# Optimization experiments

Hardware: AMD Instinct MI355X
Metric: run time of the kernel (lower is better)

## Reference

```python
import jax, jax.numpy as jnp
import numpy as np

N_NODES = 8000
N_EDGES = 64000
HEADS = 8
OUT_C = 512
NEG_SLOPE = 0.2
EPS = 1e-16


def setup_inputs() -> dict:
    key = jax.random.key(0)
    ks = jax.random.split(key, 8)
    x = jax.random.normal(ks[0], (N_NODES, 128), dtype=jnp.float32)
    edge_index = jax.random.randint(ks[1], (2, N_EDGES), 0, N_NODES, dtype=jnp.int64)
    W_gat = jax.random.normal(ks[2], (128, HEADS * OUT_C), dtype=jnp.float32) * 0.05
    b_gat = jax.random.normal(ks[3], (HEADS * OUT_C,), dtype=jnp.float32) * 0.05
    att_src = jax.random.normal(ks[4], (HEADS, OUT_C), dtype=jnp.float32) * 0.05
    att_dst = jax.random.normal(ks[5], (HEADS, OUT_C), dtype=jnp.float32) * 0.05
    W_lin = jax.random.normal(ks[6], (HEADS * OUT_C, 512), dtype=jnp.float32) * 0.02
    b_lin = jax.random.normal(ks[7], (512,), dtype=jnp.float32) * 0.02
    return {"x": x, "edge_index": edge_index, "W_gat": W_gat, "b_gat": b_gat,
            "att_src": att_src, "att_dst": att_dst, "W_lin": W_lin, "b_lin": b_lin}


def reference(x, edge_index, W_gat, b_gat, att_src, att_dst, W_lin, b_lin):
    N = x.shape[0]
    # shared linear projection (PyG GATConv single-tensor input): [N, H, C]
    h = (x @ W_gat).reshape(N, HEADS, OUT_C)
    # add self loops (PyG default add_self_loops=True)
    loop = jnp.arange(N, dtype=edge_index.dtype)
    src = jnp.concatenate([edge_index[0], loop])  # source j
    dst = jnp.concatenate([edge_index[1], loop])  # destination i
    # per-node attention logits: [N, H]
    a_src = jnp.einsum('nhc,hc->nh', h, att_src)
    a_dst = jnp.einsum('nhc,hc->nh', h, att_dst)
    # edge logits, leaky relu
    e = jax.nn.leaky_relu(a_src[src] + a_dst[dst], NEG_SLOPE)  # [E, H]
    # softmax over edges sharing a destination
    emax = jax.ops.segment_max(e, dst, num_segments=N)
    ez = jnp.exp(e - emax[dst])
    denom = jax.ops.segment_sum(ez, dst, num_segments=N)
    alpha = ez / (denom[dst] + EPS)  # [E, H]
    # weighted scatter-add of source features
    msg = h[src] * alpha[:, :, None]  # [E, H, C]
    agg = jax.ops.segment_sum(msg, dst, num_segments=N)  # [N, H, C]
    gat_out = agg.reshape(N, HEADS * OUT_C) + b_gat
    return gat_out @ W_lin + b_lin
```

## Files before the change

kernel.cpp:

```cpp
#include <hip/hip_runtime.h>
#include <hip/hip_bf16.h>
#include <type_traits>

#define NN   8000
#define NE   64000
#define NE2  72000
#define NH   8
#define OC   512
#define HC   4096
#define KIN  128
#define NOUT 512
#define YW   1024
#define NEG_SLOPE 0.2f
#define WCSK 4

using bf16 = __hip_bfloat16;
typedef float  f32x4  __attribute__((ext_vector_type(4)));
typedef __bf16 bf16x8 __attribute__((ext_vector_type(8)));

static __device__ __forceinline__ void gld_lds16(const bf16* g, bf16* l){
    __builtin_amdgcn_global_load_lds(
        (const __attribute__((address_space(1))) unsigned int*)g,
        (__attribute__((address_space(3))) unsigned int*)l, 16, 0, 0);
}

#define TCVT_NB   2048
#define VSRC_BASE 2048
#define CNT_BASE  2176
#define PHA_NB    2458

__global__ __launch_bounds__(256) void k_phaseA(
    const float* __restrict__ W_lin, const float* __restrict__ b_gat,
    const float* __restrict__ W_gat,
    const float* __restrict__ att_src, const float* __restrict__ att_dst,
    const int* __restrict__ eidx,
    bf16* __restrict__ Wl_t, float* __restrict__ b_eff,
    bf16* __restrict__ Wg_bf, float* __restrict__ v,
    int* __restrict__ counts)
{
    __shared__ __align__(16) float smem[32*33 + 32];
    const int bid = blockIdx.x;
    const int tid = threadIdx.x;

    if (bid < TCVT_NB){
        float (*t)[33] = (float(*)[33])smem;
        float* bpart = smem + 32*33;
        if (tid < 32) bpart[tid] = 0.f;
        __syncthreads();
        int tx = tid & 31, ty = tid >> 5;
        int n0 = (bid & 15) * 32, k0 = (bid >> 4) * 32;
        float pb = 0.f;
        #pragma unroll
        for (int i=0;i<4;++i){
            int k = k0 + ty + 8*i;
            float val = W_lin[(size_t)k*NOUT + n0 + tx];
            t[ty+8*i][tx] = val;
            pb = fmaf(b_gat[k], val, pb);
        }
        atomicAdd(&bpart[tx], pb);
        __syncthreads();
        #pragma unroll
        for (int i=0;i<4;++i)
            Wl_t[(size_t)(n0+ty+8*i)*HC + k0+tx] = __float2bfloat16(t[tx][ty+8*i]);
        if (tid < 32) atomicAdd(b_eff + n0 + tid, bpart[tid]);
    } else if (bid < CNT_BASE){
        int k = bid - VSRC_BASE;
        int lane = tid & 63, g = tid >> 6;
        for (int hh = g; hh < NH; hh += 4){
            const float* wp = W_gat + (size_t)k*HC + hh*OC;
            bf16*        wb = Wg_bf + (size_t)k*HC + hh*OC;
            const float* as = att_src + hh*OC;
            const float* ad = att_dst + hh*OC;
            float ss = 0.f, sd = 0.f;
            #pragma unroll
            for (int c0=0; c0<OC; c0+=64){
                float wv = wp[c0+lane];
                wb[c0+lane] = __float2bfloat16(wv);
                ss = fmaf(wv, as[c0+lane], ss);
                sd = fmaf(wv, ad[c0+lane], sd);
            }
            #pragma unroll
            for (int off=32; off; off>>=1){
                ss += __shfl_down(ss, off);
                sd += __shfl_down(sd, off);
            }
            if (lane == 0){
                v[k*16 + hh]     = ss;
                v[k*16 + 8 + hh] = sd;
            }
        }
    } else {
        int e = (bid - CNT_BASE)*256 + tid;
        if (e < NE2){
            int dst = (e < NE) ? eidx[NE + e] : (e - NE);
            atomicAdd(&counts[dst], 1);
        }
    }
}

__global__ __launch_bounds__(256) void k_phaseB(
    const bf16* __restrict__ Wl_t, const bf16* __restrict__ Wg_bf,
    float* __restrict__ partW,
    const int* __restrict__ counts, int* __restrict__ offsets)
{
    __shared__ __align__(16) bf16 sA[2][128*32];
    __shared__ __align__(16) bf16 sB[2][128*32];
    __shared__ int part[256];
    const int bid = blockIdx.x;
    const int tid = threadIdx.x;

    if (bid == 128){
        int t = tid;
        int base = t*32;
        int s = 0;
        for (int u=0;u<32;++u){ int i = base+u; if (i<NN) s += counts[i]; }
        part[t] = s;
        __syncthreads();
        for (int off=1; off<256; off<<=1){
            int vv = (t>=off) ? part[t-off] : 0;
            __syncthreads();
            part[t] += vv;
            __syncthreads();
        }
        int run = (t==0) ? 0 : part[t-1];
        for (int u=0;u<32;++u){
            int i = base+u;
            if (i<NN){ offsets[i] = run; run += counts[i]; }
        }
        if (t == 255) offsets[NN] = run;
        return;
    }

    const int head = (bid >> 2) / WCSK;
    const int sp   = (bid >> 2) % WCSK;
    const bf16* A  = Wl_t  + head*OC + sp*128;
    const bf16* BT = Wg_bf + head*OC + sp*128;
    const int lane = tid & 63;
    const int w    = tid >> 6;
    const int wm   = w >> 1, wn = w & 1;
    const int m16  = lane & 15, q = lane >> 4;
    const int m0 = (bid & 3) * 128;

    const int c0 = w*64 + lane;
    const int c1 = 256 + c0;
    const int rA0 = c0 >> 2, kA0 = (c0 & 3) * 8;
    const int rA1 = c1 >> 2, kA1 = (c1 & 3) * 8;
    const size_t gA0 = (size_t)(m0 + rA0) * HC + kA0;
    const size_t gA1 = (size_t)(m0 + rA1) * HC + kA1;
    const size_t gB0 = (size_t)rA0 * HC + kA0;
    const size_t gB1 = (size_t)rA1 * HC + kA1;

    f32x4 acc[4][4];
    #pragma unroll
    for (int i=0;i<4;++i)
        #pragma unroll
        for (int j=0;j<4;++j)
            #pragma unroll
            for (int r=0;r<4;++r) acc[i][j][r] = 0.f;

    gld_lds16(A  + gA0, sA[0] + c0*8);
    gld_lds16(A  + gA1, sA[0] + c1*8);
    gld_lds16(BT + gB0, sB[0] + c0*8);
    gld_lds16(BT + gB1, sB[0] + c1*8);
    __syncthreads();

    #pragma unroll
    for (int it = 0; it < 4; ++it){
        const int cur = it & 1, nxt = cur ^ 1;
        bf16x8 af[4], bfr[4];
        #pragma unroll
        for (int t=0;t<4;++t){
            af[t]  = *(const bf16x8*)(const void*)(sA[cur] + ((wm*64 + t*16 + m16)*32 + q*8));
            bfr[t] = *(const bf16x8*)(const void*)(sB[cur] + ((wn*64 + t*16 + m16)*32 + q*8));
        }
        if (it + 1 < 4){
            int ko = (it+1) * 32;
            gld_lds16(A  + gA0 + ko, sA[nxt] + c0*8);
            gld_lds16(A  + gA1 + ko, sA[nxt] + c1*8);
            gld_lds16(BT + gB0 + ko, sB[nxt] + c0*8);
            gld_lds16(BT + gB1 + ko, sB[nxt] + c1*8);
        }
        #pragma unroll
        for (int i=0;i<4;++i)
            #pragma unroll
            for (int j=0;j<4;++j)
                acc[i][j] = __builtin_amdgcn_mfma_f32_16x16x32_bf16(af[i], bfr[j], acc[i][j], 0, 0, 0);
        __syncthreads();
    }

    float* pout = partW + (size_t)sp*NOUT*YW + head*KIN;
    #pragma unroll
    for (int i=0;i<4;++i){
        int row_base = m0 + wm*64 + i*16 + q*4;
        #pragma unroll
        for (int j=0;j<4;++j){
            int col = wn*64 + j*16 + m16;
            #pragma unroll
            for (int r=0;r<4;++r)
                pout[(size_t)(row_base + r)*YW + col] = acc[i][j][r];
        }
    }
}

#define FILL_NB 282
#define PHC_NB  782

__global__ __launch_bounds__(256) void k_phaseC(
    const int* __restrict__ eidx, const int* __restrict__ offsets,
    int* __restrict__ cursors, int* __restrict__ esrc,
    const float* __restrict__ x, const float* __restrict__ v,
    float* __restrict__ a_src, float* __restrict__ a_dst)
{
    __shared__ __align__(16) float smem[16*132*2];
    const int bid = blockIdx.x;
    const int tid = threadIdx.x;

    if (bid < FILL_NB){
        int e = bid*256 + tid;
        if (e < NE2){
            int src, dst;
            if (e < NE){ src = eidx[e]; dst = eidx[NE+e]; } else { src = dst = e - NE; }
            int pos = atomicAdd(&cursors[dst], 1);
            esrc[offsets[dst] + pos] = src;
        }
        return;
    }
    float (*xs)[132] = (float(*)[132])smem;
    float (*vt)[132] = (float(*)[132])(smem + 16*132);
    int node0 = (bid - FILL_NB) * 16;
    {
        const float* xg = x + (size_t)node0*KIN;
        int row = tid >> 4, co = (tid & 15) * 8;
        float4 v0 = *(const float4*)(xg + row*KIN + co);
        float4 v1 = *(const float4*)(xg + row*KIN + co + 4);
        *(float4*)&xs[row][co]     = v0;
        *(float4*)&xs[row][co + 4] = v1;
    }
    {
        int base = tid*8;
        #pragma unroll
        for (int j=0;j<8;++j){
            int idx = base + j;
            vt[idx & 15][idx >> 4] = v[idx];
        }
    }
    __syncthreads();
    int ln = tid >> 4, o = tid & 15;
    float acc = 0.f;
    #pragma unroll
    for (int k0=0;k0<KIN;k0+=4){
        float4 xv = *(const float4*)&xs[ln][k0];
        float4 vv = *(const float4*)&vt[o][k0];
        acc += xv.x*vv.x + xv.y*vv.y + xv.z*vv.z + xv.w*vv.w;
    }
    int node = node0 + ln;
    if (o < 8) a_src[node*NH + o]     = acc;
    else       a_dst[node*NH + o - 8] = acc;
}

__global__ __launch_bounds__(256) void k_aggxr(const int* __restrict__ offs,
    const int* __restrict__ esrc, const float* __restrict__ a_src,
    const float* __restrict__ a_dst, const float* __restrict__ x,
    const float* __restrict__ partW, bf16* __restrict__ Y, bf16* __restrict__ WcT)
{
    int bid = blockIdx.x;
    int tid = threadIdx.x;
    if (bid >= NN/4){
        int t = (bid - NN/4)*256 + tid;
        int base = t*8;
        float s[8];
        #pragma unroll
        for (int j=0;j<8;++j) s[j] = 0.f;
        #pragma unroll
        for (int sp=0; sp<WCSK; ++sp){
            const float4* pp = (const float4*)(partW + (size_t)sp*NOUT*YW + base);
            float4 p0 = pp[0], p1 = pp[1];
            s[0]+=p0.x; s[1]+=p0.y; s[2]+=p0.z; s[3]+=p0.w;
            s[4]+=p1.x; s[5]+=p1.y; s[6]+=p1.z; s[7]+=p1.w;
        }
        bf16x8 o;
        #pragma unroll
        for (int j=0;j<8;++j) o[j] = (__bf16)s[j];
        *(bf16x8*)(void*)(WcT + base) = o;
        return;
    }
    int node = bid*4 + (tid >> 6);
    int lane = tid & 63;
    int s0 = offs[node], s1 = offs[node+1];
    int g = lane >> 3, h = lane & 7;
    float adl = a_dst[node*NH + h];
    float m = -1e30f, sum = 0.f;
    for (int e = s0 + g; e < s1; e += 8){
        float l = a_src[esrc[e]*NH + h] + adl;
        l = l > 0.f ? l : NEG_SLOPE*l;
        float mn = fmaxf(m, l);
        sum = sum*__expf(m - mn) + __expf(l - mn);
        m = mn;
    }
    #pragma unroll
    for (int d=8; d<64; d<<=1){
        float mo = __shfl_xor(m, d);
        float so = __shfl_xor(sum, d);
        float mn = fmaxf(m, mo);
        sum = sum*__expf(m - mn) + so*__expf(mo - mn);
        m = mn;
    }
    float inv = 1.f / (sum + 1e-16f);
    float acc[16];
    #pragma unroll
    for (int j=0;j<16;++j) acc[j] = 0.f;
    for (int s=s0; s<s1; ++s){
        int src = esrc[s];
        float wl = 0.f;
        if (lane < 8){
            float l = a_src[src*NH + lane] + adl;
            l = l > 0.f ? l : NEG_SLOPE*l;
            wl = __expf(l - m) * inv;
        }
        float2 xv = *(const float2*)(x + (size_t)src*KIN + lane*2);
        #pragma unroll
        for (int hh=0; hh<8; ++hh){
            float wh = __shfl(wl, hh);
            acc[hh*2]   = fmaf(wh, xv.x, acc[hh*2]);
            acc[hh*2+1] = fmaf(wh, xv.y, acc[hh*2+1]);
        }
    }
    bf16* yp = Y + (size_t)node*YW + lane*2;
    #pragma unroll
    for (int hh=0; hh<8; ++hh){
        bf16 b0 = __float2bfloat16(acc[hh*2]);
        bf16 b1 = __float2bfloat16(acc[hh*2+1]);
        ushort2 pk;
        pk.x = *(unsigned short*)&b0;
        pk.y = *(unsigned short*)&b1;
        *reinterpret_cast<ushort2*>(yp + hh*KIN) = pk;
    }
}

__global__ __launch_bounds__(256) void k_gemm64(
    const bf16* __restrict__ A, const bf16* __restrict__ BT,
    const float* __restrict__ b_eff, const float* __restrict__ b_lin,
    float* __restrict__ C, int M, int N, int K)
{
    __shared__ __align__(16) bf16 sA[2][64*32];
    __shared__ __align__(16) bf16 sB[2][128*32];
    const int tid  = threadIdx.x;
    const int lane = tid & 63;
    const int w    = tid >> 6;
    const int wm   = w >> 1, wn = w & 1;
    const int m16  = lane & 15, q = lane >> 4;
    const int m0 = blockIdx.x * 64;
    const int n0 = blockIdx.y * 128;

    const int rA = tid >> 2,  kA = (tid & 3) * 8;
    const int cB0 = tid, cB1 = 256 + tid;
    const int rB0 = cB0 >> 2, kB0 = (cB0 & 3) * 8;
    const int rB1 = cB1 >> 2, kB1 = (cB1 & 3) * 8;
    const size_t gA  = (size_t)(m0 + rA)  * K + kA;
    const size_t gB0 = (size_t)(n0 + rB0) * K + kB0;
    const size_t gB1 = (size_t)(n0 + rB1) * K + kB1;

    f32x4 acc[2][4];
    #pragma unroll
    for (int i=0;i<2;++i)
        #pragma unroll
        for (int j=0;j<4;++j)
            #pragma unroll
            for (int r=0;r<4;++r) acc[i][j][r] = 0.f;

    gld_lds16(A  + gA,  sA[0] + tid*8);
    gld_lds16(BT + gB0, sB[0] + cB0*8);
    gld_lds16(BT + gB1, sB[0] + cB1*8);
    __syncthreads();

    const int nIter = K / 32;
    for (int it = 0; it < nIter; ++it){
        const int cur = it & 1, nxt = cur ^ 1;
        bf16x8 af[2], bfr[4];
        #pragma unroll
        for (int i=0;i<2;++i)
            af[i]  = *(const bf16x8*)(const void*)(sA[cur] + ((wm*32 + i*16 + m16)*32 + q*8));
        #pragma unroll
        for (int j=0;j<4;++j)
            bfr[j] = *(const bf16x8*)(const void*)(sB[cur] + ((wn*64 + j*16 + m16)*32 + q*8));
        if (it + 1 < nIter){
            int ko = (it+1) * 32;
            gld_lds16(A  + gA  + ko, sA[nxt] + tid*8);
            gld_lds16(BT + gB0 + ko, sB[nxt] + cB0*8);
            gld_lds16(BT + gB1 + ko, sB[nxt] + cB1*8);
        }
        #pragma unroll
        for (int i=0;i<2;++i)
            #pragma unroll
            for (int j=0;j<4;++j)
                acc[i][j] = __builtin_amdgcn_mfma_f32_16x16x32_bf16(af[i], bfr[j], acc[i][j], 0, 0, 0);
        __syncthreads();
    }

    #pragma unroll
    for (int i=0;i<2;++i){
        int row_base = m0 + wm*32 + i*16 + q*4;
        #pragma unroll
        for (int j=0;j<4;++j){
            int col = n0 + wn*64 + j*16 + m16;
            float bval = b_eff[col] + b_lin[col];
            #pragma unroll
            for (int r=0;r<4;++r)
                C[(size_t)(row_base + r)*N + col] = acc[i][j][r] + bval;
        }
    }
}

extern "C" void kernel_launch(void* const* d_in, const int* in_sizes, int n_in,
                              void* d_out, int out_size, void* d_ws, size_t ws_size,
                              hipStream_t stream)
{
    const float* x       = (const float*)d_in[0];
    const int*   eidx    = (const int*)  d_in[1];
    const float* W_gat   = (const float*)d_in[2];
    const float* b_gat   = (const float*)d_in[3];
    const float* att_src = (const float*)d_in[4];
    const float* att_dst = (const float*)d_in[5];
    const float* W_lin   = (const float*)d_in[6];
    const float* b_lin   = (const float*)d_in[7];
    float* out = (float*)d_out;

    char* p = (char*)d_ws;
    auto alloc = [&](size_t bytes){ void* r = (void*)p; p += (bytes + 255) & ~(size_t)255; return r; };
    bf16*  Wg_bf  = (bf16*) alloc((size_t)KIN*HC*2);
    bf16*  Wl_t   = (bf16*) alloc((size_t)NOUT*HC*2);
    bf16*  WcT    = (bf16*) alloc((size_t)NOUT*YW*2);
    bf16*  Ybuf   = (bf16*) alloc((size_t)NN*YW*2);
    float* partW  = (float*)alloc((size_t)WCSK*NOUT*YW*4);
    float* v      = (float*)alloc((size_t)KIN*16*4);
    float* a_src  = (float*)alloc((size_t)NN*NH*4);
    float* a_dst  = (float*)alloc((size_t)NN*NH*4);
    int*   offs   = (int*)  alloc((size_t)(NN+1)*4);
    int*   esrc   = (int*)  alloc((size_t)NE2*4);
    int*   counts = (int*)  alloc((size_t)NN*4);
    int*   cursors= (int*)  alloc((size_t)NN*4);
    float* b_eff  = (float*)alloc((size_t)NOUT*4);
    if ((size_t)(p - (char*)d_ws) > ws_size) return;

    hipMemsetAsync(counts, 0, (size_t)2*NN*4 + NOUT*4, stream);
    k_phaseA<<<PHA_NB, 256, 0, stream>>>(W_lin, b_gat, W_gat, att_src, att_dst,
                                         eidx, Wl_t, b_eff, Wg_bf, v, counts);
    k_phaseB<<<129, 256, 0, stream>>>(Wl_t, Wg_bf, partW, counts, offs);
    k_phaseC<<<PHC_NB, 256, 0, stream>>>(eidx, offs, cursors, esrc, x, v, a_src, a_dst);
    k_aggxr<<<NN/4 + NOUT*YW/(8*256), 256, 0, stream>>>(offs, esrc, a_src, a_dst,
                                                        x, partW, Ybuf, WcT);
    k_gemm64<<<dim3(NN/64, NOUT/128), 256, 0, stream>>>(Ybuf, WcT, b_eff, b_lin,
                                                        out, NN, NOUT, YW);
}
```

Baseline: 151.3 us.

## Merge all phases into one cooperative persistent kernel with grid syncs

Result: slower. 464.0 us (+206.7%).

```diff
diff --git a/kernel.cpp b/kernel.cpp
--- a/kernel.cpp
+++ b/kernel.cpp
@@ -1,6 +1,9 @@
 #include <hip/hip_runtime.h>
 #include <hip/hip_bf16.h>
+#include <hip/hip_cooperative_groups.h>
 #include <type_traits>
+
+namespace cg = cooperative_groups;
 
 #define NN   8000
 #define NE   64000
@@ -14,6 +17,17 @@
 #define NEG_SLOPE 0.2f
 #define WCSK 4
 
+#define TCVT_NB   2048
+#define VSRC_BASE 2048
+#define CNT_BASE  2176
+#define P1_NB     2458
+#define P2_NB     257
+#define FILL_NB   282
+#define P3_NB     782
+#define AGG_NB    2000
+#define P4_NB     2256
+#define P5_NB     500
+
 using bf16 = __hip_bfloat16;
 typedef float  f32x4  __attribute__((ext_vector_type(4)));
 typedef __bf16 bf16x8 __attribute__((ext_vector_type(8)));
@@ -24,353 +38,34 @@
         (__attribute__((address_space(3))) unsigned int*)l, 16, 0, 0);
 }
 
-#define TCVT_NB   2048
-#define VSRC_BASE 2048
-#define CNT_BASE  2176
-#define PHA_NB    2458
-
-__global__ __launch_bounds__(256) void k_phaseA(
-    const float* __restrict__ W_lin, const float* __restrict__ b_gat,
-    const float* __restrict__ W_gat,
-    const float* __restrict__ att_src, const float* __restrict__ att_dst,
-    const int* __restrict__ eidx,
-    bf16* __restrict__ Wl_t, float* __restrict__ b_eff,
-    bf16* __restrict__ Wg_bf, float* __restrict__ v,
-    int* __restrict__ counts)
+struct Acc24 { f32x4 a[2][4]; };
+
+static __device__ __forceinline__ void gemm64x128(
+    const bf16* __restrict__ A, int lda, const bf16* __restrict__ BT, int ldb,
+    int K, bf16* sA, bf16* sB, int tid, Acc24& acc)
 {
-    __shared__ __align__(16) float smem[32*33 + 32];
-    const int bid = blockIdx.x;
-    const int tid = threadIdx.x;
-
-    if (bid < TCVT_NB){
-        float (*t)[33] = (float(*)[33])smem;
-        float* bpart = smem + 32*33;
-        if (tid < 32) bpart[tid] = 0.f;
-        __syncthreads();
-        int tx = tid & 31, ty = tid >> 5;
-        int n0 = (bid & 15) * 32, k0 = (bid >> 4) * 32;
-        float pb = 0.f;
-        #pragma unroll
-        for (int i=0;i<4;++i){
-            int k = k0 + ty + 8*i;
-            float val = W_lin[(size_t)k*NOUT + n0 + tx];
-            t[ty+8*i][tx] = val;
-            pb = fmaf(b_gat[k], val, pb);
-        }
-        atomicAdd(&bpart[tx], pb);
-        __syncthreads();
-        #pragma unroll
-        for (int i=0;i<4;++i)
-            Wl_t[(size_t)(n0+ty+8*i)*HC + k0+tx] = __float2bfloat16(t[tx][ty+8*i]);
-        if (tid < 32) atomicAdd(b_eff + n0 + tid, bpart[tid]);
-    } else if (bid < CNT_BASE){
-        int k = bid - VSRC_BASE;
-        int lane = tid & 63, g = tid >> 6;
-        for (int hh = g; hh < NH; hh += 4){
-            const float* wp = W_gat + (size_t)k*HC + hh*OC;
-            bf16*        wb = Wg_bf + (size_t)k*HC + hh*OC;
-            const float* as = att_src + hh*OC;
-            const float* ad = att_dst + hh*OC;
-            float ss = 0.f, sd = 0.f;
-            #pragma unroll
-            for (int c0=0; c0<OC; c0+=64){
-                float wv = wp[c0+lane];
-                wb[c0+lane] = __float2bfloat16(wv);
-                ss = fmaf(wv, as[c0+lane], ss);
-                sd = fmaf(wv, ad[c0+lane], sd);
-            }
-            #pragma unroll
-            for (int off=32; off; off>>=1){
-                ss += __shfl_down(ss, off);
-                sd += __shfl_down(sd, off);
-            }
-            if (lane == 0){
-                v[k*16 + hh]     = ss;
-                v[k*16 + 8 + hh] = sd;
-            }
-        }
-    } else {
-        int e = (bid - CNT_BASE)*256 + tid;
-        if (e < NE2){
-            int dst = (e < NE) ? eidx[NE + e] : (e - NE);
-            atomicAdd(&counts[dst], 1);
-        }
-    }
-}
-
-__global__ __launch_bounds__(256) void k_phaseB(
-    const bf16* __restrict__ Wl_t, const bf16* __restrict__ Wg_bf,
-    float* __restrict__ partW,
-    const int* __restrict__ counts, int* __restrict__ offsets)
-{
-    __shared__ __align__(16) bf16 sA[2][128*32];
-    __shared__ __align__(16) bf16 sB[2][128*32];
-    __shared__ int part[256];
-    const int bid = blockIdx.x;
-    const int tid = threadIdx.x;
-
-    if (bid == 128){
-        int t = tid;
-        int base = t*32;
-        int s = 0;
-        for (int u=0;u<32;++u){ int i = base+u; if (i<NN) s += counts[i]; }
-        part[t] = s;
-        __syncthreads();
-        for (int off=1; off<256; off<<=1){
-            int vv = (t>=off) ? part[t-off] : 0;
-            __syncthreads();
-            part[t] += vv;
-            __syncthreads();
-        }
-        int run = (t==0) ? 0 : part[t-1];
-        for (int u=0;u<32;++u){
-            int i = base+u;
-            if (i<NN){ offsets[i] = run; run += counts[i]; }
-        }
-        if (t == 255) offsets[NN] = run;
-        return;
-    }
-
-    const int head = (bid >> 2) / WCSK;
-    const int sp   = (bid >> 2) % WCSK;
-    const bf16* A  = Wl_t  + head*OC + sp*128;
-    const bf16* BT = Wg_bf + head*OC + sp*128;
     const int lane = tid & 63;
     const int w    = tid >> 6;
     const int wm   = w >> 1, wn = w & 1;
     const int m16  = lane & 15, q = lane >> 4;
-    const int m0 = (bid & 3) * 128;
-
-    const int c0 = w*64 + lane;
-    const int c1 = 256 + c0;
-    const int rA0 = c0 >> 2, kA0 = (c0 & 3) * 8;
-    const int rA1 = c1 >> 2, kA1 = (c1 & 3) * 8;
-    const size_t gA0 = (size_t)(m0 + rA0) * HC + kA0;
-    const size_t gA1 = (size_t)(m0 + rA1) * HC + kA1;
-    const size_t gB0 = (size_t)rA0 * HC + kA0;
-    const size_t gB1 = (size_t)rA1 * HC + kA1;
-
-    f32x4 acc[4][4];
-    #pragma unroll
-    for (int i=0;i<4;++i)
-        #pragma unroll
-        for (int j=0;j<4;++j)
-            #pragma unroll
-            for (int r=0;r<4;++r) acc[i][j][r] = 0.f;
-
-    gld_lds16(A  + gA0, sA[0] + c0*8);
-    gld_lds16(A  + gA1, sA[0] + c1*8);
-    gld_lds16(BT + gB0, sB[0] + c0*8);
-    gld_lds16(BT + gB1, sB[0] + c1*8);
-    __syncthreads();
-
-    #pragma unroll
-    for (int it = 0; it < 4; ++it){
-        const int cur = it & 1, nxt = cur ^ 1;
-        bf16x8 af[4], bfr[4];
-        #pragma unroll
-        for (int t=0;t<4;++t){
-            af[t]  = *(const bf16x8*)(const void*)(sA[cur] + ((wm*64 + t*16 + m16)*32 + q*8));
-            bfr[t] = *(const bf16x8*)(const void*)(sB[cur] + ((wn*64 + t*16 + m16)*32 + q*8));
-        }
-        if (it + 1 < 4){
-            int ko = (it+1) * 32;
-            gld_lds16(A  + gA0 + ko, sA[nxt] + c0*8);
-            gld_lds16(A  + gA1 + ko, sA[nxt] + c1*8);
-            gld_lds16(BT + gB0 + ko, sB[nxt] + c0*8);
-            gld_lds16(BT + gB1 + ko, sB[nxt] + c1*8);
-        }
-        #pragma unroll
-        for (int i=0;i<4;++i)
-            #pragma unroll
-            for (int j=0;j<4;++j)
-                acc[i][j] = __builtin_amdgcn_mfma_f32_16x16x32_bf16(af[i], bfr[j], acc[i][j], 0, 0, 0);
-        __syncthreads();
-    }
-
-    float* pout = partW + (size_t)sp*NOUT*YW + head*KIN;
-    #pragma unroll
-    for (int i=0;i<4;++i){
-        int row_base = m0 + wm*64 + i*16 + q*4;
-        #pragma unroll
-        for (int j=0;j<4;++j){
-            int col = wn*64 + j*16 + m16;
-            #pragma unroll
-            for (int r=0;r<4;++r)
-                pout[(size_t)(row_base + r)*YW + col] = acc[i][j][r];
-        }
-    }
-}
-
-#define FILL_NB 282
-#define PHC_NB  782
-
-__global__ __launch_bounds__(256) void k_phaseC(
-    const int* __restrict__ eidx, const int* __restrict__ offsets,
-    int* __restrict__ cursors, int* __restrict__ esrc,
-    const float* __restrict__ x, const float* __restrict__ v,
-    float* __restrict__ a_src, float* __restrict__ a_dst)
-{
-    __shared__ __align__(16) float smem[16*132*2];
-    const int bid = blockIdx.x;
-    const int tid = threadIdx.x;
-
-    if (bid < FILL_NB){
-        int e = bid*256 + tid;
-        if (e < NE2){
-            int src, dst;
-            if (e < NE){ src = eidx[e]; dst = eidx[NE+e]; } else { src = dst = e - NE; }
-            int pos = atomicAdd(&cursors[dst], 1);
-            esrc[offsets[dst] + pos] = src;
-        }
-        return;
-    }
-    float (*xs)[132] = (float(*)[132])smem;
-    float (*vt)[132] = (float(*)[132])(smem + 16*132);
-    int node0 = (bid - FILL_NB) * 16;
-    {
-        const float* xg = x + (size_t)node0*KIN;
-        int row = tid >> 4, co = (tid & 15) * 8;
-        float4 v0 = *(const float4*)(xg + row*KIN + co);
-        float4 v1 = *(const float4*)(xg + row*KIN + co + 4);
-        *(float4*)&xs[row][co]     = v0;
-        *(float4*)&xs[row][co + 4] = v1;
-    }
-    {
-        int base = tid*8;
-        #pragma unroll
-        for (int j=0;j<8;++j){
-            int idx = base + j;
-            vt[idx & 15][idx >> 4] = v[idx];
-        }
-    }
-    __syncthreads();
-    int ln = tid >> 4, o = tid & 15;
-    float acc = 0.f;
-    #pragma unroll
-    for (int k0=0;k0<KIN;k0+=4){
-        float4 xv = *(const float4*)&xs[ln][k0];
-        float4 vv = *(const float4*)&vt[o][k0];
-        acc += xv.x*vv.x + xv.y*vv.y + xv.z*vv.z + xv.w*vv.w;
-    }
-    int node = node0 + ln;
-    if (o < 8) a_src[node*NH + o]     = acc;
-    else       a_dst[node*NH + o - 8] = acc;
-}
-
-__global__ __launch_bounds__(256) void k_aggxr(const int* __restrict__ offs,
-    const int* __restrict__ esrc, const float* __restrict__ a_src,
-    const float* __restrict__ a_dst, const float* __restrict__ x,
-    const float* __restrict__ partW, bf16* __restrict__ Y, bf16* __restrict__ WcT)
-{
-    int bid = blockIdx.x;
-    int tid = threadIdx.x;
-    if (bid >= NN/4){
-        int t = (bid - NN/4)*256 + tid;
-        int base = t*8;
-        float s[8];
-        #pragma unroll
-        for (int j=0;j<8;++j) s[j] = 0.f;
-        #pragma unroll
-        for (int sp=0; sp<WCSK; ++sp){
-            const float4* pp = (const float4*)(partW + (size_t)sp*NOUT*YW + base);
-            float4 p0 = pp[0], p1 = pp[1];
-            s[0]+=p0.x; s[1]+=p0.y; s[2]+=p0.z; s[3]+=p0.w;
-            s[4]+=p1.x; s[5]+=p1.y; s[6]+=p1.z; s[7]+=p1.w;
-        }
-        bf16x8 o;
-        #pragma unroll
-        for (int j=0;j<8;++j) o[j] = (__bf16)s[j];
-        *(bf16x8*)(void*)(WcT + base) = o;
-        return;
-    }
-    int node = bid*4 + (tid >> 6);
-    int lane = tid & 63;
-    int s0 = offs[node], s1 = offs[node+1];
-    int g = lane >> 3, h = lane & 7;
-    float adl = a_dst[node*NH + h];
-    float m = -1e30f, sum = 0.f;
-    for (int e = s0 + g; e < s1; e += 8){
-        float l = a_src[esrc[e]*NH + h] + adl;
-        l = l > 0.f ? l : NEG_SLOPE*l;
-        float mn = fmaxf(m, l);
-        sum = sum*__expf(m - mn) + __expf(l - mn);
-        m = mn;
-    }
-    #pragma unroll
-    for (int d=8; d<64; d<<=1){
-        float mo = __shfl_xor(m, d);
-        float so = __shfl_xor(sum, d);
-        float mn = fmaxf(m, mo);
-        sum = sum*__expf(m - mn) + so*__expf(mo - mn);
-        m = mn;
-    }
-    float inv = 1.f / (sum + 1e-16f);
-    float acc[16];
-    #pragma unroll
-    for (int j=0;j<16;++j) acc[j] = 0.f;
-    for (int s=s0; s<s1; ++s){
-        int src = esrc[s];
-        float wl = 0.f;
-        if (lane < 8){
-            float l = a_src[src*NH + lane] + adl;
-            l = l > 0.f ? l : NEG_SLOPE*l;
-            wl = __expf(l - m) * inv;
-        }
-        float2 xv = *(const float2*)(x + (size_t)src*KIN + lane*2);
-        #pragma unroll
-        for (int hh=0; hh<8; ++hh){
-            float wh = __shfl(wl, hh);
-            acc[hh*2]   = fmaf(wh, xv.x, acc[hh*2]);
-            acc[hh*2+1] = fmaf(wh, xv.y, acc[hh*2+1]);
-        }
-    }
-    bf16* yp = Y + (size_t)node*YW + lane*2;
-    #pragma unroll
-    for (int hh=0; hh<8; ++hh){
-        bf16 b0 = __float2bfloat16(acc[hh*2]);
-        bf16 b1 = __float2bfloat16(acc[hh*2+1]);
-        ushort2 pk;
-        pk.x = *(unsigned short*)&b0;
-        pk.y = *(unsigned short*)&b1;
-        *reinterpret_cast<ushort2*>(yp + hh*KIN) = pk;
-    }
-}
-
-__global__ __launch_bounds__(256) void k_gemm64(
-    const bf16* __restrict__ A, const bf16* __restrict__ BT,
-    const float* __restrict__ b_eff, const float* __restrict__ b_lin,
-    float* __restrict__ C, int M, int N, int K)
-{
-    __shared__ __align__(16) bf16 sA[2][64*32];
-    __shared__ __align__(16) bf16 sB[2][128*32];
-    const int tid  = threadIdx.x;
-    const int lane = tid & 63;
-    const int w    = tid >> 6;
-    const int wm   = w >> 1, wn = w & 1;
-    const int m16  = lane & 15, q = lane >> 4;
-    const int m0 = blockIdx.x * 64;
-    const int n0 = blockIdx.y * 128;
-
     const int rA = tid >> 2,  kA = (tid & 3) * 8;
     const int cB0 = tid, cB1 = 256 + tid;
     const int rB0 = cB0 >> 2, kB0 = (cB0 & 3) * 8;
     const int rB1 = cB1 >> 2, kB1 = (cB1 & 3) * 8;
-    const size_t gA  = (size_t)(m0 + rA)  * K + kA;
-    const size_t gB0 = (size_t)(n0 + rB0) * K + kB0;
-    const size_t gB1 = (size_t)(n0 + rB1) * K + kB1;
-
-    f32x4 acc[2][4];
+    const size_t gA  = (size_t)rA  * lda + kA;
+    const size_t gB0 = (size_t)rB0 * ldb + kB0;
+    const size_t gB1 = (size_t)rB1 * ldb + kB1;
+
     #pragma unroll
     for (int i=0;i<2;++i)
         #pragma unroll
         for (int j=0;j<4;++j)
             #pragma unroll
-            for (int r=0;r<4;++r) acc[i][j][r] = 0.f;
-
-    gld_lds16(A  + gA,  sA[0] + tid*8);
-    gld_lds16(BT + gB0, sB[0] + cB0*8);
-    gld_lds16(BT + gB1, sB[0] + cB1*8);
+            for (int r=0;r<4;++r) acc.a[i][j][r] = 0.f;
+
+    gld_lds16(A  + gA,  sA + tid*8);
+    gld_lds16(BT + gB0, sB + cB0*8);
+    gld_lds16(BT + gB1, sB + cB1*8);
     __syncthreads();
 
     const int nIter = K / 32;
@@ -379,34 +74,301 @@
         bf16x8 af[2], bfr[4];
         #pragma unroll
         for (int i=0;i<2;++i)
-            af[i]  = *(const bf16x8*)(const void*)(sA[cur] + ((wm*32 + i*16 + m16)*32 + q*8));
+            af[i]  = *(const bf16x8*)(const void*)(sA + cur*64*32 + ((wm*32 + i*16 + m16)*32 + q*8));
         #pragma unroll
         for (int j=0;j<4;++j)
-            bfr[j] = *(const bf16x8*)(const void*)(sB[cur] + ((wn*64 + j*16 + m16)*32 + q*8));
+            bfr[j] = *(const bf16x8*)(const void*)(sB + cur*128*32 + ((wn*64 + j*16 + m16)*32 + q*8));
         if (it + 1 < nIter){
             int ko = (it+1) * 32;
-            gld_lds16(A  + gA  + ko, sA[nxt] + tid*8);
-            gld_lds16(BT + gB0 + ko, sB[nxt] + cB0*8);
-            gld_lds16(BT + gB1 + ko, sB[nxt] + cB1*8);
+            gld_lds16(A  + gA  + ko, sA + nxt*64*32 + tid*8);
+            gld_lds16(BT + gB0 + ko, sB + nxt*128*32 + cB0*8);
+            gld_lds16(BT + gB1 + ko, sB + nxt*128*32 + cB1*8);
         }
         #pragma unroll
         for (int i=0;i<2;++i)
             #pragma unroll
             for (int j=0;j<4;++j)
-                acc[i][j] = __builtin_amdgcn_mfma_f32_16x16x32_bf16(af[i], bfr[j], acc[i][j], 0, 0, 0);
+                acc.a[i][j] = __builtin_amdgcn_mfma_f32_16x16x32_bf16(af[i], bfr[j], acc.a[i][j], 0, 0, 0);
         __syncthreads();
     }
-
-    #pragma unroll
-    for (int i=0;i<2;++i){
-        int row_base = m0 + wm*32 + i*16 + q*4;
+}
+
+__global__ __launch_bounds__(256, 4) void k_mega(
+    const float* __restrict__ x, const int* __restrict__ eidx,
+    const float* __restrict__ W_gat, const float* __restrict__ b_gat,
+    const float* __restrict__ att_src, const float* __restrict__ att_dst,
+    const float* __restrict__ W_lin, const float* __restrict__ b_lin,
+    float* __restrict__ out,
+    bf16* __restrict__ Wl_t, bf16* __restrict__ Wg_bf,
+    bf16* __restrict__ WcT, bf16* __restrict__ Ybuf,
+    float* __restrict__ partW, float* __restrict__ v,
+    float* __restrict__ a_src, float* __restrict__ a_dst,
+    int* __restrict__ offs, int* __restrict__ esrc,
+    int* __restrict__ zero_base)
+{
+    cg::grid_group grid = cg::this_grid();
+    __shared__ __align__(16) char smem_raw[24576];
+    int*   counts  = zero_base;
+    int*   cursors = zero_base + NN;
+    float* b_eff   = (float*)(zero_base + 2*NN);
+    const int tid = threadIdx.x;
+    const int nb  = gridDim.x;
+
+    for (int i = blockIdx.x*256 + tid; i < 2*NN + NOUT; i += nb*256)
+        zero_base[i] = 0;
+    grid.sync();
+
+    for (int vb = blockIdx.x; vb < P1_NB; vb += nb){
+        if (vb < TCVT_NB){
+            float (*t)[33] = (float(*)[33])smem_raw;
+            float* bpart = (float*)smem_raw + 32*33;
+            if (tid < 32) bpart[tid] = 0.f;
+            __syncthreads();
+            int tx = tid & 31, ty = tid >> 5;
+            int n0 = (vb & 15)*32, k0 = (vb >> 4)*32;
+            float pb = 0.f;
+            #pragma unroll
+            for (int i=0;i<4;++i){
+                int k = k0 + ty + 8*i;
+                float val = W_lin[(size_t)k*NOUT + n0 + tx];
+                t[ty+8*i][tx] = val;
+                pb = fmaf(b_gat[k], val, pb);
+            }
+            atomicAdd(&bpart[tx], pb);
+            __syncthreads();
+            #pragma unroll
+            for (int i=0;i<4;++i)
+                Wl_t[(size_t)(n0+ty+8*i)*HC + k0+tx] = __float2bfloat16(t[tx][ty+8*i]);
+            if (tid < 32) atomicAdd(b_eff + n0 + tid, bpart[tid]);
+            __syncthreads();
+        } else if (vb < CNT_BASE){
+            int k = vb - VSRC_BASE;
+            int lane = tid & 63, g = tid >> 6;
+            for (int hh = g; hh < NH; hh += 4){
+                const float* wp = W_gat + (size_t)k*HC + hh*OC;
+                bf16*        wb = Wg_bf + (size_t)k*HC + hh*OC;
+                const float* as = att_src + hh*OC;
+                const float* ad = att_dst + hh*OC;
+                float ss = 0.f, sd = 0.f;
+                #pragma unroll
+                for (int c0=0; c0<OC; c0+=64){
+                    float wv = wp[c0+lane];
+                    wb[c0+lane] = __float2bfloat16(wv);
+                    ss = fmaf(wv, as[c0+lane], ss);
+                    sd = fmaf(wv, ad[c0+lane], sd);
+                }
+                #pragma unroll
+                for (int off=32; off; off>>=1){
+                    ss += __shfl_down(ss, off);
+                    sd += __shfl_down(sd, off);
+                }
+                if (lane == 0){
+                    v[k*16 + hh]     = ss;
+                    v[k*16 + 8 + hh] = sd;
+                }
+            }
+        } else {
+            int e = (vb - CNT_BASE)*256 + tid;
+            if (e < NE2){
+                int dst = (e < NE) ? eidx[NE + e] : (e - NE);
+                atomicAdd(&counts[dst], 1);
+            }
+        }
+    }
+    grid.sync();
+
+    for (int vb = blockIdx.x; vb < P2_NB; vb += nb){
+        if (vb < 256){
+            bf16* sA = (bf16*)smem_raw;
+            bf16* sB = (bf16*)(smem_raw + 8192);
+            int head = vb >> 5, sp = (vb >> 3) & 3, mt = vb & 7;
+            const bf16* A  = Wl_t  + head*OC + sp*128 + (size_t)(mt*64)*HC;
+            const bf16* BT = Wg_bf + head*OC + sp*128;
+            Acc24 acc;
+            gemm64x128(A, HC, BT, HC, 128, sA, sB, tid, acc);
+            const int lane = tid & 63;
+            const int w = tid >> 6, wm = w >> 1, wn = w & 1;
+            const int m16 = lane & 15, q = lane >> 4;
+            float* pout = partW + (size_t)sp*NOUT*YW + head*KIN;
+            #pragma unroll
+            for (int i=0;i<2;++i){
+                int o_base = mt*64 + wm*32 + i*16 + q*4;
+                #pragma unroll
+                for (int j=0;j<4;++j){
+                    int col = wn*64 + j*16 + m16;
+                    #pragma unroll
+                    for (int r=0;r<4;++r)
+                        pout[(size_t)(o_base + r)*YW + col] = acc.a[i][j][r];
+                }
+            }
+        } else {
+            int* part = (int*)smem_raw;
+            int t = tid;
+            int base = t*32;
+            int s = 0;
+            for (int u=0;u<32;++u){ int i = base+u; if (i<NN) s += counts[i]; }
+            part[t] = s;
+            __syncthreads();
+            for (int off=1; off<256; off<<=1){
+                int vv = (t>=off) ? part[t-off] : 0;
+                __syncthreads();
+                part[t] += vv;
+                __syncthreads();
+            }
+            int run = (t==0) ? 0 : part[t-1];
+            for (int u=0;u<32;++u){
+                int i = base+u;
+                if (i<NN){ offs[i] = run; run += counts[i]; }
+            }
+            if (t == 255) offs[NN] = run;
+            __syncthreads();
+        }
+    }
+    grid.sync();
+
+    for (int vb = blockIdx.x; vb < P3_NB; vb += nb){
+        if (vb < FILL_NB){
+            int e = vb*256 + tid;
+            if (e < NE2){
+                int src, dst;
+                if (e < NE){ src = eidx[e]; dst = eidx[NE+e]; } else { src = dst = e - NE; }
+                int pos = atomicAdd(&cursors[dst], 1);
+                esrc[offs[dst] + pos] = src;
+            }
+        } else {
+            float (*xs)[132] = (float(*)[132])smem_raw;
+            float (*vt)[132] = (float(*)[132])((float*)smem_raw + 16*132);
+            int node0 = (vb - FILL_NB) * 16;
+            {
+                const float* xg = x + (size_t)node0*KIN;
+                int row = tid >> 4, co = (tid & 15) * 8;
+                float4 v0 = *(const float4*)(xg + row*KIN + co);
+                float4 v1 = *(const float4*)(xg + row*KIN + co + 4);
+                *(float4*)&xs[row][co]     = v0;
+                *(float4*)&xs[row][co + 4] = v1;
+            }
+            {
+                int base = tid*8;
+                #pragma unroll
+                for (int j=0;j<8;++j){
+                    int idx = base + j;
+                    vt[idx & 15][idx >> 4] = v[idx];
+                }
+            }
+            __syncthreads();
+            int ln = tid >> 4, o = tid & 15;
+            float acc = 0.f;
+            #pragma unroll
+            for (int k0=0;k0<KIN;k0+=4){
+                float4 xv = *(const float4*)&xs[ln][k0];
+                float4 vv = *(const float4*)&vt[o][k0];
+                acc += xv.x*vv.x + xv.y*vv.y + xv.z*vv.z + xv.w*vv.w;
+            }
+            int node = node0 + ln;
+            if (o < 8) a_src[node*NH + o]     = acc;
+            else       a_dst[node*NH + o - 8] = acc;
+            __syncthreads();
+        }
+    }
+    grid.sync();
+
+    for (int vb = blockIdx.x; vb < P4_NB; vb += nb){
+        if (vb >= AGG_NB){
+            int t = (vb - AGG_NB)*256 + tid;
+            int base = t*8;
+            float s[8];
+            #pragma unroll
+            for (int j=0;j<8;++j) s[j] = 0.f;
+            #pragma unroll
+            for (int sp=0; sp<WCSK; ++sp){
+                const float4* pp = (const float4*)(partW + (size_t)sp*NOUT*YW + base);
+                float4 p0 = pp[0], p1 = pp[1];
+                s[0]+=p0.x; s[1]+=p0.y; s[2]+=p0.z; s[3]+=p0.w;
+                s[4]+=p1.x; s[5]+=p1.y; s[6]+=p1.z; s[7]+=p1.w;
+            }
+            bf16x8 o;
+            #pragma unroll
+            for (int j=0;j<8;++j) o[j] = (__bf16)s[j];
+            *(bf16x8*)(void*)(WcT + base) = o;
+        } else {
+            int node = vb*4 + (tid >> 6);
+            int lane = tid & 63;
+            int s0 = offs[node], s1 = offs[node+1];
+            int g = lane >> 3, h = lane & 7;
+            float adl = a_dst[node*NH + h];
+            float m = -1e30f, sum = 0.f;
+            for (int e = s0 + g; e < s1; e += 8){
+                float l = a_src[esrc[e]*NH + h] + adl;
+                l = l > 0.f ? l : NEG_SLOPE*l;
+                float mn = fmaxf(m, l);
+                sum = sum*__expf(m - mn) + __expf(l - mn);
+                m = mn;
+            }
+            #pragma unroll
+            for (int d=8; d<64; d<<=1){
+                float mo = __shfl_xor(m, d);
+                float so = __shfl_xor(sum, d);
+                float mn = fmaxf(m, mo);
+                sum = sum*__expf(m - mn) + so*__expf(mo - mn);
+                m = mn;
+            }
+            float inv = 1.f / (sum + 1e-16f);
+            float acc[16];
+            #pragma unroll
+            for (int j=0;j<16;++j) acc[j] = 0.f;
+            for (int s=s0; s<s1; ++s){
+                int src = esrc[s];
+                float wl = 0.f;
+                if (lane < 8){
+                    float l = a_src[src*NH + lane] + adl;
+                    l = l > 0.f ? l : NEG_SLOPE*l;
+                    wl = __expf(l - m) * inv;
+                }
+                float2 xv = *(const float2*)(x + (size_t)src*KIN + lane*2);
+                #pragma unroll
+                for (int hh=0; hh<8; ++hh){
+                    float wh = __shfl(wl, hh);
+                    acc[hh*2]   = fmaf(wh, xv.x, acc[hh*2]);
+                    acc[hh*2+1] = fmaf(wh, xv.y, acc[hh*2+1]);
+                }
+            }
+            bf16* yp = Ybuf + (size_t)node*YW + lane*2;
+            #pragma unroll
+            for (int hh=0; hh<8; ++hh){
+                bf16 b0 = __float2bfloat16(acc[hh*2]);
+                bf16 b1 = __float2bfloat16(acc[hh*2+1]);
+                ushort2 pk;
+                pk.x = *(unsigned short*)&b0;
+                pk.y = *(unsigned short*)&b1;
+                *reinterpret_cast<ushort2*>(yp + hh*KIN) = pk;
+            }
+        }
+    }
+    grid.sync();
+
+    for (int vb = blockIdx.x; vb < P5_NB; vb += nb){
+        bf16* sA = (bf16*)smem_raw;
+        bf16* sB = (bf16*)(smem_raw + 8192);
+        int m0 = (vb % 125) * 64;
+        int n0 = (vb / 125) * 128;
+        const bf16* A  = Ybuf + (size_t)m0*YW;
+        const bf16* BT = WcT  + (size_t)n0*YW;
+        Acc24 acc;
+        gemm64x128(A, YW, BT, YW, YW, sA, sB, tid, acc);
+        const int lane = tid & 63;
+        const int w = tid >> 6, wm = w >> 1, wn = w & 1;
+        const int m16 = lane & 15, q = lane >> 4;
         #pragma unroll
-        for (int j=0;j<4;++j){
-            int col = n0 + wn*64 + j*16 + m16;
-            float bval = b_eff[col] + b_lin[col];
-            #pragma unroll
-            for (int r=0;r<4;++r)
-                C[(size_t)(row_base + r)*N + col] = acc[i][j][r] + bval;
+        for (int i=0;i<2;++i){
+            int row_base = m0 + wm*32 + i*16 + q*4;
+            #pragma unroll
+            for (int j=0;j<4;++j){
+                int col = n0 + wn*64 + j*16 + m16;
+                float bval = b_eff[col] + b_lin[col];
+                #pragma unroll
+                for (int r=0;r<4;++r)
+                    out[(size_t)(row_base + r)*NOUT + col] = acc.a[i][j][r] + bval;
+            }
         }
     }
 }
@@ -437,18 +399,22 @@
     float* a_dst  = (float*)alloc((size_t)NN*NH*4);
     int*   offs   = (int*)  alloc((size_t)(NN+1)*4);
     int*   esrc   = (int*)  alloc((size_t)NE2*4);
-    int*   counts = (int*)  alloc((size_t)NN*4);
-    int*   cursors= (int*)  alloc((size_t)NN*4);
-    float* b_eff  = (float*)alloc((size_t)NOUT*4);
+    int*   zb     = (int*)  alloc((size_t)(2*NN + NOUT)*4);
     if ((size_t)(p - (char*)d_ws) > ws_size) return;
 
-    hipMemsetAsync(counts, 0, (size_t)2*NN*4 + NOUT*4, stream);
-    k_phaseA<<<PHA_NB, 256, 0, stream>>>(W_lin, b_gat, W_gat, att_src, att_dst,
-                                         eidx, Wl_t, b_eff, Wg_bf, v, counts);
-    k_phaseB<<<129, 256, 0, stream>>>(Wl_t, Wg_bf, partW, counts, offs);
-    k_phaseC<<<PHC_NB, 256, 0, stream>>>(eidx, offs, cursors, esrc, x, v, a_src, a_dst);
-    k_aggxr<<<NN/4 + NOUT*YW/(8*256), 256, 0, stream>>>(offs, esrc, a_src, a_dst,
-                                                        x, partW, Ybuf, WcT);
-    k_gemm64<<<dim3(NN/64, NOUT/128), 256, 0, stream>>>(Ybuf, WcT, b_eff, b_lin,
-                                                        out, NN, NOUT, YW);
+    int maxB = 0;
+    hipOccupancyMaxActiveBlocksPerMultiprocessor(&maxB, k_mega, 256, 0);
+    int nblocks = maxB * 256;
+    if (nblocks > 1024) nblocks = 1024;
+    if (nblocks < 256)  nblocks = (maxB > 0) ? maxB*256 : 256;
+
+    void* args[] = {
+        (void*)&x, (void*)&eidx, (void*)&W_gat, (void*)&b_gat,
+        (void*)&att_src, (void*)&att_dst, (void*)&W_lin, (void*)&b_lin,
+        (void*)&out, (void*)&Wl_t, (void*)&Wg_bf, (void*)&WcT, (void*)&Ybuf,
+        (void*)&partW, (void*)&v, (void*)&a_src, (void*)&a_dst,
+        (void*)&offs, (void*)&esrc, (void*)&zb
+    };
+    hipLaunchCooperativeKernel((const void*)k_mega, dim3(nblocks), dim3(256),
+                               args, 0, stream);
 }
```

## Drop split-K in weight-combine GEMM and share a 64x128 MFMA tile helper

Applied to the files above, without the earlier changes.

Measured after the change: 147.5 us. 1.03x faster.

```diff
diff --git a/kernel.cpp b/kernel.cpp
--- a/kernel.cpp
+++ b/kernel.cpp
@@ -12,7 +12,6 @@
 #define NOUT 512
 #define YW   1024
 #define NEG_SLOPE 0.2f
-#define WCSK 4
 
 using bf16 = __hip_bfloat16;
 typedef float  f32x4  __attribute__((ext_vector_type(4)));
@@ -22,6 +21,61 @@
     __builtin_amdgcn_global_load_lds(
         (const __attribute__((address_space(1))) unsigned int*)g,
         (__attribute__((address_space(3))) unsigned int*)l, 16, 0, 0);
+}
+
+struct Acc24 { f32x4 a[2][4]; };
+
+static __device__ __forceinline__ void gemm64x128(
+    const bf16* __restrict__ A, int lda, const bf16* __restrict__ BT, int ldb,
+    int K, bf16* sA, bf16* sB, int tid, Acc24& acc)
+{
+    const int lane = tid & 63;
+    const int w    = tid >> 6;
+    const int wm   = w >> 1, wn = w & 1;
+    const int m16  = lane & 15, q = lane >> 4;
+    const int rA = tid >> 2,  kA = (tid & 3) * 8;
+    const int cB0 = tid, cB1 = 256 + tid;
+    const int rB0 = cB0 >> 2, kB0 = (cB0 & 3) * 8;
+    const int rB1 = cB1 >> 2, kB1 = (cB1 & 3) * 8;
+    const size_t gA  = (size_t)rA  * lda + kA;
+    const size_t gB0 = (size_t)rB0 * ldb + kB0;
+    const size_t gB1 = (size_t)rB1 * ldb + kB1;
+
+    #pragma unroll
+    for (int i=0;i<2;++i)
+        #pragma unroll
+        for (int j=0;j<4;++j)
+            #pragma unroll
+            for (int r=0;r<4;++r) acc.a[i][j][r] = 0.f;
+
+    gld_lds16(A  + gA,  sA + tid*8);
+    gld_lds16(BT + gB0, sB + cB0*8);
+    gld_lds16(BT + gB1, sB + cB1*8);
+    __syncthreads();
+
+    const int nIter = K / 32;
+    for (int it = 0; it < nIter; ++it){
+        const int cur = it & 1, nxt = cur ^ 1;
+        bf16x8 af[2], bfr[4];
+        #pragma unroll
+        for (int i=0;i<2;++i)
+            af[i]  = *(const bf16x8*)(const void*)(sA + cur*64*32 + ((wm*32 + i*16 + m16)*32 + q*8));
+        #pragma unroll
+        for (int j=0;j<4;++j)
+            bfr[j] = *(const bf16x8*)(const void*)(sB + cur*128*32 + ((wn*64 + j*16 + m16)*32 + q*8));
+        if (it + 1 < nIter){
+            int ko = (it+1) * 32;
+            gld_lds16(A  + gA  + ko, sA + nxt*64*32 + tid*8);
+            gld_lds16(BT + gB0 + ko, sB + nxt*128*32 + cB0*8);
+            gld_lds16(BT + gB1 + ko, sB + nxt*128*32 + cB1*8);
+        }
+        #pragma unroll
+        for (int i=0;i<2;++i)
+            #pragma unroll
+            for (int j=0;j<4;++j)
+                acc.a[i][j] = __builtin_amdgcn_mfma_f32_16x16x32_bf16(af[i], bfr[j], acc.a[i][j], 0, 0, 0);
+        __syncthreads();
+    }
 }
 
 #define TCVT_NB   2048
@@ -100,16 +154,15 @@
 
 __global__ __launch_bounds__(256) void k_phaseB(
     const bf16* __restrict__ Wl_t, const bf16* __restrict__ Wg_bf,
-    float* __restrict__ partW,
+    bf16* __restrict__ WcT,
     const int* __restrict__ counts, int* __restrict__ offsets)
 {
-    __shared__ __align__(16) bf16 sA[2][128*32];
-    __shared__ __align__(16) bf16 sB[2][128*32];
+    __shared__ __align__(16) char smem_raw[24576];
     __shared__ int part[256];
     const int bid = blockIdx.x;
     const int tid = threadIdx.x;
 
-    if (bid == 128){
+    if (bid == 64){
         int t = tid;
         int base = t*32;
         int s = 0;
@@ -131,73 +184,25 @@
         return;
     }
 
-    const int head = (bid >> 2) / WCSK;
-    const int sp   = (bid >> 2) % WCSK;
-    const bf16* A  = Wl_t  + head*OC + sp*128;
-    const bf16* BT = Wg_bf + head*OC + sp*128;
+    bf16* sA = (bf16*)smem_raw;
+    bf16* sB = (bf16*)(smem_raw + 8192);
+    const int head = bid >> 3, mt = bid & 7;
+    const bf16* A  = Wl_t  + head*OC + (size_t)(mt*64)*HC;
+    const bf16* BT = Wg_bf + head*OC;
+    Acc24 acc;
+    gemm64x128(A, HC, BT, HC, OC, sA, sB, tid, acc);
     const int lane = tid & 63;
-    const int w    = tid >> 6;
-    const int wm   = w >> 1, wn = w & 1;
-    const int m16  = lane & 15, q = lane >> 4;
-    const int m0 = (bid & 3) * 128;
-
-    const int c0 = w*64 + lane;
-    const int c1 = 256 + c0;
-    const int rA0 = c0 >> 2, kA0 = (c0 & 3) * 8;
-    const int rA1 = c1 >> 2, kA1 = (c1 & 3) * 8;
-    const size_t gA0 = (size_t)(m0 + rA0) * HC + kA0;
-    const size_t gA1 = (size_t)(m0 + rA1) * HC + kA1;
-    const size_t gB0 = (size_t)rA0 * HC + kA0;
-    const size_t gB1 = (size_t)rA1 * HC + kA1;
-
-    f32x4 acc[4][4];
-    #pragma unroll
-    for (int i=0;i<4;++i)
-        #pragma unroll
-        for (int j=0;j<4;++j)
-            #pragma unroll
-            for (int r=0;r<4;++r) acc[i][j][r] = 0.f;
-
-    gld_lds16(A  + gA0, sA[0] + c0*8);
-    gld_lds16(A  + gA1, sA[0] + c1*8);
-    gld_lds16(BT + gB0, sB[0] + c0*8);
-    gld_lds16(BT + gB1, sB[0] + c1*8);
-    __syncthreads();
-
-    #pragma unroll
-    for (int it = 0; it < 4; ++it){
-        const int cur = it & 1, nxt = cur ^ 1;
-        bf16x8 af[4], bfr[4];
-        #pragma unroll
-        for (int t=0;t<4;++t){
-            af[t]  = *(const bf16x8*)(const void*)(sA[cur] + ((wm*64 + t*16 + m16)*32 + q*8));
-            bfr[t] = *(const bf16x8*)(const void*)(sB[cur] + ((wn*64 + t*16 + m16)*32 + q*8));
-        }
-        if (it + 1 < 4){
-            int ko = (it+1) * 32;
-            gld_lds16(A  + gA0 + ko, sA[nxt] + c0*8);
-            gld_lds16(A  + gA1 + ko, sA[nxt] + c1*8);
-            gld_lds16(BT + gB0 + ko, sB[nxt] + c0*8);
-            gld_lds16(BT + gB1 + ko, sB[nxt] + c1*8);
-        }
-        #pragma unroll
-        for (int i=0;i<4;++i)
-            #pragma unroll
-            for (int j=0;j<4;++j)
-                acc[i][j] = __builtin_amdgcn_mfma_f32_16x16x32_bf16(af[i], bfr[j], acc[i][j], 0, 0, 0);
-        __syncthreads();
-    }
-
-    float* pout = partW + (size_t)sp*NOUT*YW + head*KIN;
-    #pragma unroll
-    for (int i=0;i<4;++i){
-        int row_base = m0 + wm*64 + i*16 + q*4;
+    const int w = tid >> 6, wm = w >> 1, wn = w & 1;
+    const int m16 = lane & 15, q = lane >> 4;
+    #pragma unroll
+    for (int i=0;i<2;++i){
+        int o_base = mt*64 + wm*32 + i*16 + q*4;
         #pragma unroll
         for (int j=0;j<4;++j){
-            int col = wn*64 + j*16 + m16;
+            int col = head*KIN + wn*64 + j*16 + m16;
             #pragma unroll
             for (int r=0;r<4;++r)
-                pout[(size_t)(row_base + r)*YW + col] = acc[i][j][r];
+                WcT[(size_t)(o_base + r)*YW + col] = __float2bfloat16(acc.a[i][j][r]);
         }
     }
 }
@@ -258,34 +263,13 @@
     else       a_dst[node*NH + o - 8] = acc;
 }
 
-__global__ __launch_bounds__(256) void k_aggxr(const int* __restrict__ offs,
+__global__ __launch_bounds__(256) void k_agg(const int* __restrict__ offs,
     const int* __restrict__ esrc, const float* __restrict__ a_src,
     const float* __restrict__ a_dst, const float* __restrict__ x,
-    const float* __restrict__ partW, bf16* __restrict__ Y, bf16* __restrict__ WcT)
-{
-    int bid = blockIdx.x;
-    int tid = threadIdx.x;
-    if (bid >= NN/4){
-        int t = (bid - NN/4)*256 + tid;
-        int base = t*8;
-        float s[8];
-        #pragma unroll
-        for (int j=0;j<8;++j) s[j] = 0.f;
-        #pragma unroll
-        for (int sp=0; sp<WCSK; ++sp){
-            const float4* pp = (const float4*)(partW + (size_t)sp*NOUT*YW + base);
-            float4 p0 = pp[0], p1 = pp[1];
-            s[0]+=p0.x; s[1]+=p0.y; s[2]+=p0.z; s[3]+=p0.w;
-            s[4]+=p1.x; s[5]+=p1.y; s[6]+=p1.z; s[7]+=p1.w;
-        }
-        bf16x8 o;
-        #pragma unroll
-        for (int j=0;j<8;++j) o[j] = (__bf16)s[j];
-        *(bf16x8*)(void*)(WcT + base) = o;
-        return;
-    }
-    int node = bid*4 + (tid >> 6);
-    int lane = tid & 63;
+    bf16* __restrict__ Y)
+{
+    int node = blockIdx.x*4 + (threadIdx.x >> 6);
+    int lane = threadIdx.x & 63;
     int s0 = offs[node], s1 = offs[node+1];
     int g = lane >> 3, h = lane & 7;
     float adl = a_dst[node*NH + h];
@@ -340,63 +324,19 @@
 __global__ __launch_bounds__(256) void k_gemm64(
     const bf16* __restrict__ A, const bf16* __restrict__ BT,
     const float* __restrict__ b_eff, const float* __restrict__ b_lin,
-    float* __restrict__ C, int M, int N, int K)
-{
-    __shared__ __align__(16) bf16 sA[2][64*32];
-    __shared__ __align__(16) bf16 sB[2][128*32];
-    const int tid  = threadIdx.x;
+    float* __restrict__ C)
+{
+    __shared__ __align__(16) char smem_raw[24576];
+    bf16* sA = (bf16*)smem_raw;
+    bf16* sB = (bf16*)(smem_raw + 8192);
+    const int tid = threadIdx.x;
+    int m0 = blockIdx.x * 64;
+    int n0 = blockIdx.y * 128;
+    Acc24 acc;
+    gemm64x128(A + (size_t)m0*YW, YW, BT + (size_t)n0*YW, YW, YW, sA, sB, tid, acc);
     const int lane = tid & 63;
-    const int w    = tid >> 6;
-    const int wm   = w >> 1, wn = w & 1;
-    const int m16  = lane & 15, q = lane >> 4;
-    const int m0 = blockIdx.x * 64;
-    const int n0 = blockIdx.y * 128;
-
-    const int rA = tid >> 2,  kA = (tid & 3) * 8;
-    const int cB0 = tid, cB1 = 256 + tid;
-    const int rB0 = cB0 >> 2, kB0 = (cB0 & 3) * 8;
-    const int rB1 = cB1 >> 2, kB1 = (cB1 & 3) * 8;
-    const size_t gA  = (size_t)(m0 + rA)  * K + kA;
-    const size_t gB0 = (size_t)(n0 + rB0) * K + kB0;
-    const size_t gB1 = (size_t)(n0 + rB1) * K + kB1;
-
-    f32x4 acc[2][4];
-    #pragma unroll
-    for (int i=0;i<2;++i)
-        #pragma unroll
-        for (int j=0;j<4;++j)
-            #pragma unroll
-            for (int r=0;r<4;++r) acc[i][j][r] = 0.f;
-
-    gld_lds16(A  + gA,  sA[0] + tid*8);
-    gld_lds16(BT + gB0, sB[0] + cB0*8);
-    gld_lds16(BT + gB1, sB[0] + cB1*8);
-    __syncthreads();
-
-    const int nIter = K / 32;
-    for (int it = 0; it < nIter; ++it){
-        const int cur = it & 1, nxt = cur ^ 1;
-        bf16x8 af[2], bfr[4];
-        #pragma unroll
-        for (int i=0;i<2;++i)
-            af[i]  = *(const bf16x8*)(const void*)(sA[cur] + ((wm*32 + i*16 + m16)*32 + q*8));
-        #pragma unroll
-        for (int j=0;j<4;++j)
-            bfr[j] = *(const bf16x8*)(const void*)(sB[cur] + ((wn*64 + j*16 + m16)*32 + q*8));
-        if (it + 1 < nIter){
-            int ko = (it+1) * 32;
-            gld_lds16(A  + gA  + ko, sA[nxt] + tid*8);
-            gld_lds16(BT + gB0 + ko, sB[nxt] + cB0*8);
-            gld_lds16(BT + gB1 + ko, sB[nxt] + cB1*8);
-        }
-        #pragma unroll
-        for (int i=0;i<2;++i)
-            #pragma unroll
-            for (int j=0;j<4;++j)
-                acc[i][j] = __builtin_amdgcn_mfma_f32_16x16x32_bf16(af[i], bfr[j], acc[i][j], 0, 0, 0);
-        __syncthreads();
-    }
-
+    const int w = tid >> 6, wm = w >> 1, wn = w & 1;
+    const int m16 = lane & 15, q = lane >> 4;
     #pragma unroll
     for (int i=0;i<2;++i){
         int row_base = m0 + wm*32 + i*16 + q*4;
@@ -406,7 +346,7 @@
             float bval = b_eff[col] + b_lin[col];
             #pragma unroll
             for (int r=0;r<4;++r)
-                C[(size_t)(row_base + r)*N + col] = acc[i][j][r] + bval;
+                C[(size_t)(row_base + r)*NOUT + col] = acc.a[i][j][r] + bval;
         }
     }
 }
@@ -431,7 +371,6 @@
     bf16*  Wl_t   = (bf16*) alloc((size_t)NOUT*HC*2);
     bf16*  WcT    = (bf16*) alloc((size_t)NOUT*YW*2);
     bf16*  Ybuf   = (bf16*) alloc((size_t)NN*YW*2);
-    float* partW  = (float*)alloc((size_t)WCSK*NOUT*YW*4);
     float* v      = (float*)alloc((size_t)KIN*16*4);
     float* a_src  = (float*)alloc((size_t)NN*NH*4);
     float* a_dst  = (float*)alloc((size_t)NN*NH*4);
@@ -445,10 +384,8 @@
     hipMemsetAsync(counts, 0, (size_t)2*NN*4 + NOUT*4, stream);
     k_phaseA<<<PHA_NB, 256, 0, stream>>>(W_lin, b_gat, W_gat, att_src, att_dst,
                                          eidx, Wl_t, b_eff, Wg_bf, v, counts);
-    k_phaseB<<<129, 256, 0, stream>>>(Wl_t, Wg_bf, partW, counts, offs);
+    k_phaseB<<<65, 256, 0, stream>>>(Wl_t, Wg_bf, WcT, counts, offs);
     k_phaseC<<<PHC_NB, 256, 0, stream>>>(eidx, offs, cursors, esrc, x, v, a_src, a_dst);
-    k_aggxr<<<NN/4 + NOUT*YW/(8*256), 256, 0, stream>>>(offs, esrc, a_src, a_dst,
-                                                        x, partW, Ybuf, WcT);
-    k_gemm64<<<dim3(NN/64, NOUT/128), 256, 0, stream>>>(Ybuf, WcT, b_eff, b_lin,
-                                                        out, NN, NOUT, YW);
-}
+    k_agg<<<NN/4, 256, 0, stream>>>(offs, esrc, a_src, a_dst, x, Ybuf);
+    k_gemm64<<<dim3(NN/64, NOUT/128), 256, 0, stream>>>(Ybuf, WcT, b_eff, b_lin, out);
+}
```
